# Performance work log

Measured on AMD Instinct MI355X. Metric: run time of the kernel, lower is better.

Reference implementation:

```python
import jax, jax.numpy as jnp
import numpy as np

SIGMA = 10
POPULATIONS = 2
LR = 0.001


def _normalize(L, prior):
    # clamp then normalize over populations (logsumexp across the population axis)
    O = L.shape[1]
    L = jnp.clip(L, -5.0, 0.0)
    lse = jax.nn.logsumexp(L.reshape(POPULATIONS, -1, O), axis=0)  # (in/P, O)
    L = L - jnp.tile(lse, (POPULATIONS, 1))
    prior = jnp.clip(prior, -5.0, 0.0)
    prior = prior - jax.nn.logsumexp(prior)
    return L, prior


def _forward(x, L, prior):
    B, T, IN = x.shape
    O = L.shape[1]
    L, prior = _normalize(L, prior)  # matches normalize_probs() in __init__

    # membrane potential: OR of spikes over trailing window of SIGMA steps
    xb = x.astype(bool)
    pot = xb
    for s in range(1, SIGMA):  # fixed small loop (sigma=10)
        pot = pot | jnp.pad(xb, ((0, 0), (s, 0), (0, 0)))[:, :T, :]

    tpre0 = jnp.full((B, IN), -T, dtype=jnp.int32)
    tpost0 = jnp.full((B, O), jnp.iinfo(jnp.int32).max, dtype=jnp.int32)
    base_key = jax.random.key(42)

    pot_T = jnp.transpose(pot, (1, 0, 2))  # (T,B,IN)
    x_T = jnp.transpose(xb, (1, 0, 2))

    def step(carry, inp):
        L, prior, tpre, tpost, t = carry
        pot_t, x_t = inp
        potf = pot_t.astype(L.dtype)
        logits = potf @ L + prior  # (B,O), logits <= 0 so exp is safe
        # torch: softmax(exp(logits)).multinomial == categorical with logits=exp(logits)
        key = jax.random.fold_in(base_key, t)
        widx = jax.random.categorical(key, jnp.exp(logits), axis=-1)  # (B,)
        win = jax.nn.one_hot(widx, O, dtype=L.dtype)
        # trace updates happen BEFORE STDP, as in the torch code
        tpre = jnp.where(x_t, 0, tpre - 1)
        tpost = jnp.where(win > 0, 0, tpost - 1)
        ltp = (tpre >= -SIGMA).astype(L.dtype)
        ltd = (tpre < -SIGMA).astype(L.dtype)
        post = (tpost < 0).astype(L.dtype)
        m_ltp = jnp.einsum('bi,bo->io', ltp, win) / B
        m_ltd = jnp.einsum('bi,bo->io', ltd, win) / B
        m_pp = jnp.einsum('bi,bo->io', potf, post) / B
        decay = (t + 1).astype(L.dtype)  # lr_decay_inverse starts at 1
        # dw = (5 e^{-L} - 1) * LTP.mean - LTD.mean - pre_post.mean ; LTD was negated
        dw = (5.0 * jnp.exp(-L) - 1.0) * m_ltp + m_ltd - m_pp
        L2 = L + (LR / decay) * dw
        wm = jnp.mean(win, axis=0)
        db = (-5.0 * prior - 1.0) * wm - (1.0 - wm)
        p2 = prior + (LR / decay) * db
        L2, p2 = _normalize(L2, p2)
        return (L2, p2, tpre, tpost, t + 1), None

    (Lf, pf, _, _, _), _ = jax.lax.scan(
        step, (L, prior, tpre0, tpost0, jnp.int32(0)), (pot_T, x_T))
    return jnp.concatenate([Lf.reshape(-1), pf])


def setup_inputs() -> dict:
    key = jax.random.key(0)
    k1, k2, k3 = jax.random.split(key, 3)
    B, T, IN, O = 256, 200, 1568, 100
    x = jax.random.randint(k1, (B, T, IN), 0, 2, dtype=jnp.int32)
    log_likelihood = jax.random.uniform(k2, (IN, O), dtype=jnp.float32) * -1.0 - 1.0
    log_prior = jax.random.uniform(k3, (O,), dtype=jnp.float32) * -1.0 - 1.0
    return {"x": x, "log_likelihood": log_likelihood, "log_prior": log_prior}


def reference(x, log_likelihood, log_prior):
    return _forward(x, log_likelihood, log_prior)
```

## Files before the change

kernel.cpp:

```cpp
#include <hip/hip_runtime.h>
#include <stdint.h>

#define BB 256
#define TT 200
#define INN 1568
#define OO 100
#define PAIRS 784
#define NHALF 12800
#define NBLK 240
#define UNITS 686
#define ROWSTRIDE (4 * INN)

typedef unsigned long long u64;
typedef __attribute__((ext_vector_type(4))) int v4i;

typedef const __attribute__((address_space(1))) uint32_t* gas_p;
typedef __attribute__((address_space(3))) uint32_t* las_p;
#define GLD16(g, l) __builtin_amdgcn_global_load_lds((gas_p)(g), (las_p)(l), 16, 0, 0)

__device__ __forceinline__ void tf_round(uint32_t& x0, uint32_t& x1, int r) {
    x0 += x1;
    x1 = (x1 << r) | (x1 >> (32 - r));
    x1 ^= x0;
}

__device__ __forceinline__ void threefry(uint32_t k0, uint32_t k1,
                                         uint32_t x0, uint32_t x1,
                                         uint32_t& o0, uint32_t& o1) {
    uint32_t k2 = k0 ^ k1 ^ 0x1BD11BDAu;
    x0 += k0; x1 += k1;
    tf_round(x0,x1,13); tf_round(x0,x1,15); tf_round(x0,x1,26); tf_round(x0,x1,6);
    x0 += k1; x1 += k2 + 1u;
    tf_round(x0,x1,17); tf_round(x0,x1,29); tf_round(x0,x1,16); tf_round(x0,x1,24);
    x0 += k2; x1 += k0 + 2u;
    tf_round(x0,x1,13); tf_round(x0,x1,15); tf_round(x0,x1,26); tf_round(x0,x1,6);
    x0 += k0; x1 += k1 + 3u;
    tf_round(x0,x1,17); tf_round(x0,x1,29); tf_round(x0,x1,16); tf_round(x0,x1,24);
    x0 += k1; x1 += k2 + 4u;
    tf_round(x0,x1,13); tf_round(x0,x1,15); tf_round(x0,x1,26); tf_round(x0,x1,6);
    o0 = x0 + k2; o1 = x1 + k0 + 5u;
}

struct FusedSM {
    u64 rows[8][16][64];
    u64 wp[8][8][128];
    u64 potC[8][2][8][10];
    u64 ltpC[8][2][8][10];
    uint32_t cntR[8][8][16];
};
struct FwSM { uint32_t wl32[TT * 65]; int fwl[BB]; };
union SMem { FusedSM f; FwSM w; };

__device__ __forceinline__ void gridsync(uint32_t* c) {
    __syncthreads();
    if (threadIdx.x == 0) {
        __threadfence();
        __hip_atomic_fetch_add(c, 1u, __ATOMIC_ACQ_REL, __HIP_MEMORY_SCOPE_AGENT);
        while (__hip_atomic_load(c, __ATOMIC_ACQUIRE, __HIP_MEMORY_SCOPE_AGENT)
               < (uint32_t)NBLK)
            __builtin_amdgcn_s_sleep(8);
        __threadfence();
    }
    __syncthreads();
}

__global__ __launch_bounds__(512, 1) void k_mono(
        const int* __restrict__ x,
        const float* __restrict__ L0,
        const float* __restrict__ p0arr,
        uint32_t* __restrict__ syncc,
        uint8_t* __restrict__ widx,
        uint32_t* __restrict__ cntg,
        u64* __restrict__ winbits,
        u64* __restrict__ postbits,
        u64* __restrict__ bitB,
        float* __restrict__ outL,
        float* __restrict__ outp) {
    __shared__ SMem sm;
    __shared__ uint32_t smclaim;
    const int tid = threadIdx.x;
    const int bid = blockIdx.x;

    {
        int idx = bid * 214 + tid;
        if (tid < 214 && idx < TT * BB) {
            int t = idx >> 8, b = idx & 255;
            uint32_t fk0, fk1;
            threefry(0u, 42u, 0u, (uint32_t)t, fk0, fk1);
            uint32_t bestkey = 0u;
            int bo = 0;
            int nbase = b * OO;
            for (int o = 0; o < OO; ++o) {
                uint32_t n = (uint32_t)(nbase + o);
                uint32_t lo = (n < NHALF) ? n : n - NHALF;
                uint32_t v0, v1;
                threefry(fk0, fk1, lo, lo + NHALF, v0, v1);
                uint32_t bits = (n < NHALF) ? v0 : v1;
                uint32_t key = bits >> 9;
                if (key > bestkey) { bestkey = key; bo = o; }
            }
            widx[idx] = (uint8_t)bo;
        }
    }
    gridsync(&syncc[0]);

    if (bid < 100) {
        const uint32_t* wsrc = (const uint32_t*)widx;
        for (int g = tid; g < TT * 64; g += 512)
            sm.w.wl32[(g >> 6) * 65 + (g & 63)] = wsrc[g];
        __syncthreads();
        int o = bid;
        if (tid < 64) {
            int f0 = 255, f1 = 255, f2 = 255, f3 = 255;
            for (int t = 0; t < TT; ++t) {
                uint32_t w4 = sm.w.wl32[t * 65 + tid];
                if (((w4      ) & 255u) == (uint32_t)o && f0 == 255) f0 = t;
                if (((w4 >>  8) & 255u) == (uint32_t)o && f1 == 255) f1 = t;
                if (((w4 >> 16) & 255u) == (uint32_t)o && f2 == 255) f2 = t;
                if (((w4 >> 24) & 255u) == (uint32_t)o && f3 == 255) f3 = t;
            }
            sm.w.fwl[4 * tid + 0] = f0; sm.w.fwl[4 * tid + 1] = f1;
            sm.w.fwl[4 * tid + 2] = f2; sm.w.fwl[4 * tid + 3] = f3;
        }
        __syncthreads();
        if (tid < TT) {
            int t = tid;
            u64 wbA[4], pbA[4];
            uint32_t c = 0;
            #pragma unroll
            for (int k = 0; k < 4; ++k) {
                u64 wacc = 0, pacc = 0;
                for (int q2 = 0; q2 < 16; ++q2) {
                    uint32_t w4 = sm.w.wl32[t * 65 + k * 16 + q2];
                    #pragma unroll
                    for (int j = 0; j < 4; ++j) {
                        int bl = q2 * 4 + j;
                        bool win = (((w4 >> (8 * j)) & 255u) == (uint32_t)o);
                        c += win ? 1u : 0u;
                        bool post = (sm.w.fwl[k * 64 + q2 * 4 + j] < t) && !win;
                        u64 bit = 1ull << bl;
                        if (win)  wacc |= bit;
                        if (post) pacc |= bit;
                    }
                }
                wbA[k] = wacc; pbA[k] = pacc;
            }
            size_t base = (size_t)(t * OO + o) * 4;
            #pragma unroll
            for (int k = 0; k < 4; ++k) {
                winbits[base + k] = wbA[k];
                postbits[base + k] = pbA[k];
            }
            cntg[t * OO + o] = c;
        }
        __syncthreads();
    }

    {
        const v4i* xp = (const v4i*)x;
        for (;;) {
            __syncthreads();
            if (tid == 0)
                smclaim = __hip_atomic_fetch_add(&syncc[2], 1u, __ATOMIC_RELAXED,
                                                 __HIP_MEMORY_SCOPE_AGENT);
            __syncthreads();
            uint32_t u = smclaim;
            if (u >= 200u) break;
            int wb = u & 3, tc = u >> 2;
            u64 acc[4][4];
            #pragma unroll
            for (int q = 0; q < 4; ++q)
                #pragma unroll
                for (int c = 0; c < 4; ++c) acc[q][c] = 0;
            bool x4 = (tid < 32);
            for (int blb = 0; blb < 64; blb += 4) {
                v4i v[4][3];
                v4i vt[4];
                #pragma unroll
                for (int s4 = 0; s4 < 4; ++s4) {
                    size_t base = ((size_t)((wb * 64 + blb + s4) * TT + tc * 4)) * 392;
                    #pragma unroll
                    for (int q = 0; q < 3; ++q)
                        v[s4][q] = __builtin_nontemporal_load(&xp[base + tid + q * 512]);
                    if (x4)
                        vt[s4] = __builtin_nontemporal_load(&xp[base + tid + 1536]);
                }
                #pragma unroll
                for (int s4 = 0; s4 < 4; ++s4) {
                    u64 bit = 1ull << (blb + s4);
                    #pragma unroll
                    for (int q = 0; q < 3; ++q) {
                        if (v[s4][q].x) acc[q][0] |= bit;
                        if (v[s4][q].y) acc[q][1] |= bit;
                        if (v[s4][q].z) acc[q][2] |= bit;
                        if (v[s4][q].w) acc[q][3] |= bit;
                    }
                    if (x4) {
                        if (vt[s4].x) acc[3][0] |= bit;
                        if (vt[s4].y) acc[3][1] |= bit;
                        if (vt[s4].z) acc[3][2] |= bit;
                        if (vt[s4].w) acc[3][3] |= bit;
                    }
                }
            }
            #pragma unroll
            for (int q = 0; q < 4; ++q) {
                if (q == 3 && !x4) continue;
                int p = tid + q * 512;
                int tp = (p >= 1176) ? 3 : (p >= 784) ? 2 : (p >= 392) ? 1 : 0;
                int iq = p - tp * 392;
                u64* dst = bitB + ((size_t)((tc * 4 + tp) * 4 + wb)) * INN + iq * 4;
                dst[0] = acc[q][0]; dst[1] = acc[q][1];
                dst[2] = acc[q][2]; dst[3] = acc[q][3];
            }
        }
    }
    gridsync(&syncc[1]);

    {
        const int wv = tid >> 6, lane = tid & 63;
        int u = bid + NBLK * wv;
        if (u > UNITS) return;
        if (u == UNITS) {
            int l = lane;
            bool has2 = (l + 64) < OO;
            float pa = p0arr[l];
            float pb = has2 ? p0arr[l + 64] : -1e30f;
            auto norm = [&]() {
                pa = fminf(fmaxf(pa, -5.0f), 0.0f);
                if (has2) pb = fminf(fmaxf(pb, -5.0f), 0.0f);
                float mx = has2 ? fmaxf(pa, pb) : pa;
                #pragma unroll
                for (int s = 32; s > 0; s >>= 1) mx = fmaxf(mx, __shfl_xor(mx, s, 64));
                float smv = expf(pa - mx) + (has2 ? expf(pb - mx) : 0.0f);
                #pragma unroll
                for (int s = 32; s > 0; s >>= 1) smv += __shfl_xor(smv, s, 64);
                float lse = logf(smv) + mx;
                pa -= lse;
                if (has2) pb -= lse;
            };
            norm();
            for (int t = 0; t < TT; ++t) {
                float eta = 0.001f / (float)(t + 1);
                float wma = (float)cntg[t * OO + l] * (1.0f / 256.0f);
                pa += eta * ((-5.0f * pa - 1.0f) * wma - (1.0f - wma));
                if (has2) {
                    float wmb = (float)cntg[t * OO + l + 64] * (1.0f / 256.0f);
                    pb += eta * ((-5.0f * pb - 1.0f) * wmb - (1.0f - wmb));
                }
                norm();
            }
            outp[l] = pa;
            if (has2) outp[l + 64] = pb;
            return;
        }

        const int pg = u % 98, og = u / 98;
        const int p0 = pg * 8, o0 = og * 16;
        const int pl = lane & 7, ol = lane >> 3;
        const int oA = o0 + ol, oB = oA + 8;
        const int i0 = p0 + pl, i1 = i0 + PAIRS;
        const bool actA = (oA < OO), actB = (oB < OO);

        const int e0 = (lane & 31) * 2;
        const int wk0 = e0 >> 3, wpl0 = e0 & 7;
        const u64* rowg = bitB + (size_t)((wk0 & 3) * INN + (wk0 >> 2) * PAIRS
                                          + p0 + wpl0);
        const int lw = lane & 31;
        const u64* wpg = (lane < 32) ? winbits : postbits;
        const bool wpact = (o0 + (lw >> 1)) < OO;
        const bool cntact = (lane < 8) && ((o0 + (lane & 3) * 4) < OO);

        auto issueG = [&](int G) {
            int r0 = 2 * G;
            {
                int rr = r0 + (lane >> 5); if (rr > TT - 1) rr = TT - 1;
                GLD16(rowg + (size_t)rr * ROWSTRIDE,
                      (las_p)&sm.f.rows[wv][r0 & 15][0]);
            }
            {
                int rr = r0; if (rr > TT - 1) rr = TT - 1;
                if (wpact)
                    GLD16(wpg + ((size_t)rr * OO + o0) * 4 + 2 * lw,
                          (las_p)&sm.f.wp[wv][r0 & 7][0]);
            }
            {
                int rr = r0 + 1; if (rr > TT - 1) rr = TT - 1;
                if (wpact)
                    GLD16(wpg + ((size_t)rr * OO + o0) * 4 + 2 * lw,
                          (las_p)&sm.f.wp[wv][(r0 + 1) & 7][0]);
            }
            {
                if (cntact) {
                    int rr = r0 + (lane >> 2); if (rr > TT - 1) rr = TT - 1;
                    GLD16(cntg + (size_t)rr * OO + o0 + (lane & 3) * 4,
                          (las_p)&sm.f.cntR[wv][r0 & 7][0]);
                }
            }
        };

        float aA = actA ? L0[(size_t)i0 * OO + oA] : -1.0f;
        float bA = actA ? L0[(size_t)i1 * OO + oA] : -1.0f;
        float aB = actB ? L0[(size_t)i0 * OO + oB] : -1.0f;
        float bB = actB ? L0[(size_t)i1 * OO + oB] : -1.0f;
        {
            aA = fminf(fmaxf(aA, -5.0f), 0.0f);
            bA = fminf(fmaxf(bA, -5.0f), 0.0f);
            float m = fmaxf(aA, bA), mn = fminf(aA, bA);
            float lse = __logf(1.0f + __expf(mn - m)) + m;
            aA -= lse; bA -= lse;
            aB = fminf(fmaxf(aB, -5.0f), 0.0f);
            bB = fminf(fmaxf(bB, -5.0f), 0.0f);
            float m2 = fmaxf(aB, bB), mn2 = fminf(aB, bB);
            float lse2 = __logf(1.0f + __expf(mn2 - m2)) + m2;
            aB -= lse2; bB -= lse2;
        }

        auto chainstep = [&](int t, int sp) {
            int s = t & 7;
            const u64* wpS = &sm.f.wp[wv][s][0];
            const u64* P = sm.f.potC[wv][sp][pl];
            const u64* Lt = sm.f.ltpC[wv][sp][pl];
            u64 P0 = P[0], P1 = P[1], P2 = P[2], P3 = P[3];
            u64 P4 = P[4], P5 = P[5], P6 = P[6], P7 = P[7];
            u64 Q0 = Lt[0], Q1 = Lt[1], Q2 = Lt[2], Q3 = Lt[3];
            u64 Q4 = Lt[4], Q5 = Lt[5], Q6 = Lt[6], Q7 = Lt[7];
            float eta = 0.001f / (float)(t + 1);
            {
                u64 W0 = wpS[ol*4+0], W1 = wpS[ol*4+1], W2 = wpS[ol*4+2], W3 = wpS[ol*4+3];
                u64 S0 = wpS[64+ol*4+0], S1 = wpS[64+ol*4+1], S2 = wpS[64+ol*4+2], S3 = wpS[64+ol*4+3];
                float cw = (float)sm.f.cntR[wv][s][ol];
                float lt0 = (float)(__popcll(Q0&W0)+__popcll(Q1&W1)+__popcll(Q2&W2)+__popcll(Q3&W3));
                float lt1 = (float)(__popcll(Q4&W0)+__popcll(Q5&W1)+__popcll(Q6&W2)+__popcll(Q7&W3));
                float pp0 = (float)(__popcll(P0&S0)+__popcll(P1&S1)+__popcll(P2&S2)+__popcll(P3&S3));
                float pp1 = (float)(__popcll(P4&S0)+__popcll(P5&S1)+__popcll(P6&S2)+__popcll(P7&S3));
                float dw0 = (5.0f*__expf(-aA) - 1.0f)*(lt0*(1.0f/256.0f))
                          + (cw - lt0 - pp0)*(1.0f/256.0f);
                float dw1 = (5.0f*__expf(-bA) - 1.0f)*(lt1*(1.0f/256.0f))
                          + (cw - lt1 - pp1)*(1.0f/256.0f);
                aA += eta*dw0; bA += eta*dw1;
                aA = fminf(fmaxf(aA,-5.0f),0.0f);
                bA = fminf(fmaxf(bA,-5.0f),0.0f);
                float m = fmaxf(aA,bA), mn = fminf(aA,bA);
                float lse = __logf(1.0f + __expf(mn-m)) + m;
                aA -= lse; bA -= lse;
            }
            {
                u64 W0 = wpS[(ol+8)*4+0], W1 = wpS[(ol+8)*4+1], W2 = wpS[(ol+8)*4+2], W3 = wpS[(ol+8)*4+3];
                u64 S0 = wpS[64+(ol+8)*4+0], S1 = wpS[64+(ol+8)*4+1], S2 = wpS[64+(ol+8)*4+2], S3 = wpS[64+(ol+8)*4+3];
                float cw = (float)sm.f.cntR[wv][s][ol+8];
                float lt0 = (float)(__popcll(Q0&W0)+__popcll(Q1&W1)+__popcll(Q2&W2)+__popcll(Q3&W3));
                float lt1 = (float)(__popcll(Q4&W0)+__popcll(Q5&W1)+__popcll(Q6&W2)+__popcll(Q7&W3));
                float pp0 = (float)(__popcll(P0&S0)+__popcll(P1&S1)+__popcll(P2&S2)+__popcll(P3&S3));
                float pp1 = (float)(__popcll(P4&S0)+__popcll(P5&S1)+__popcll(P6&S2)+__popcll(P7&S3));
                float dw0 = (5.0f*__expf(-aB) - 1.0f)*(lt0*(1.0f/256.0f))
                          + (cw - lt0 - pp0)*(1.0f/256.0f);
                float dw1 = (5.0f*__expf(-bB) - 1.0f)*(lt1*(1.0f/256.0f))
                          + (cw - lt1 - pp1)*(1.0f/256.0f);
                aB += eta*dw0; bB += eta*dw1;
                aB = fminf(fmaxf(aB,-5.0f),0.0f);
                bB = fminf(fmaxf(bB,-5.0f),0.0f);
                float m = fmaxf(aB,bB), mn = fminf(aB,bB);
                float lse = __logf(1.0f + __expf(mn-m)) + m;
                aB -= lse; bB -= lse;
            }
        };

        issueG(0);
        issueG(1);
        for (int I = 0; I < 100; ++I) {
            issueG(I + 2);
            asm volatile("s_waitcnt vmcnt(8)" ::: "memory");
            int b0 = 2 * I;
            u64 com = 0;
            #pragma unroll
            for (int j = 8; j >= 0; --j) {
                int r = b0 - j; r = (r < 0) ? 0 : r;
                com |= sm.f.rows[wv][r & 15][lane];
            }
            int r9 = b0 - 9;   r9 = (r9 < 0) ? 0 : r9;
            int r10 = b0 - 10; r10 = (r10 < 0) ? 0 : r10;
            u64 v9  = sm.f.rows[wv][r9 & 15][lane];
            u64 v10 = sm.f.rows[wv][r10 & 15][lane];
            u64 vt2 = sm.f.rows[wv][(b0 + 1) & 15][lane];
            u64 pot1 = com | v9;
            u64 pot2 = com | vt2;
            sm.f.potC[wv][0][lane & 7][lane >> 3] = pot1;
            sm.f.potC[wv][1][lane & 7][lane >> 3] = pot2;
            sm.f.ltpC[wv][0][lane & 7][lane >> 3] = pot1 | v10;
            sm.f.ltpC[wv][1][lane & 7][lane >> 3] = pot2 | v9;
            asm volatile("s_waitcnt lgkmcnt(0)" ::: "memory");
            chainstep(b0, 0);
            chainstep(b0 + 1, 1);
        }
        if (actA) {
            outL[(size_t)i0 * OO + oA] = aA;
            outL[(size_t)i1 * OO + oA] = bA;
        }
        if (actB) {
            outL[(size_t)i0 * OO + oB] = aB;
            outL[(size_t)i1 * OO + oB] = bB;
        }
    }
}

extern "C" void kernel_launch(void* const* d_in, const int* in_sizes, int n_in,
                              void* d_out, int out_size, void* d_ws, size_t ws_size,
                              hipStream_t stream) {
    const int*   x  = (const int*)d_in[0];
    const float* L0 = (const float*)d_in[1];
    const float* p0 = (const float*)d_in[2];
    float* out = (float*)d_out;

    char* ws = (char*)d_ws;
    size_t off = 0;
    auto alloc = [&](size_t bytes) -> void* {
        off = (off + 255) & ~(size_t)255;
        void* p = ws + off;
        off += bytes;
        return p;
    };
    uint32_t* syncc    = (uint32_t*)alloc(256);
    uint8_t*  widx     = (uint8_t*) alloc((size_t)TT * BB);
    uint32_t* cntg     = (uint32_t*)alloc((size_t)TT * OO * 4);
    u64*      winbits  = (u64*)     alloc((size_t)TT * OO * 4 * 8);
    u64*      postbits = (u64*)     alloc((size_t)TT * OO * 4 * 8);
    u64*      bitB     = (u64*)     alloc((size_t)TT * 4 * INN * 8);
    (void)ws_size;

    hipMemsetAsync(syncc, 0, 256, stream);
    hipLaunchKernelGGL(k_mono, dim3(NBLK), dim3(512), 0, stream,
                       x, L0, p0, syncc, widx, cntg, winbits, postbits, bitB,
                       out, out + (size_t)INN * OO);
}
```

Before: 689.1 us.

## Restructure STDP chain phase to one element per thread with dedicated loader wave

```diff
diff --git a/kernel.cpp b/kernel.cpp
--- a/kernel.cpp
+++ b/kernel.cpp
@@ -8,7 +8,6 @@
 #define PAIRS 784
 #define NHALF 12800
 #define NBLK 240
-#define UNITS 686
 #define ROWSTRIDE (4 * INN)
 
 typedef unsigned long long u64;
@@ -41,23 +40,24 @@
     o0 = x0 + k2; o1 = x1 + k0 + 5u;
 }
 
-struct FusedSM {
-    u64 rows[8][16][64];
-    u64 wp[8][8][128];
-    u64 potC[8][2][8][10];
-    u64 ltpC[8][2][8][10];
-    uint32_t cntR[8][8][16];
+struct DSM {
+    u64 rowsR[32][128];
+    u64 winR[8][128];
+    u64 postR[8][128];
+    uint32_t cntR[8][32];
+    u64 potC[2][16][10];
+    u64 ltpC[2][16][10];
 };
 struct FwSM { uint32_t wl32[TT * 65]; int fwl[BB]; };
-union SMem { FusedSM f; FwSM w; };
-
-__device__ __forceinline__ void gridsync(uint32_t* c) {
+union SMem { DSM d; FwSM w; };
+
+__device__ __forceinline__ void gridsync(uint32_t* c, uint32_t target) {
     __syncthreads();
     if (threadIdx.x == 0) {
         __threadfence();
         __hip_atomic_fetch_add(c, 1u, __ATOMIC_ACQ_REL, __HIP_MEMORY_SCOPE_AGENT);
         while (__hip_atomic_load(c, __ATOMIC_ACQUIRE, __HIP_MEMORY_SCOPE_AGENT)
-               < (uint32_t)NBLK)
+               < target)
             __builtin_amdgcn_s_sleep(8);
         __threadfence();
     }
@@ -81,9 +81,9 @@
     const int tid = threadIdx.x;
     const int bid = blockIdx.x;
 
-    {
-        int idx = bid * 214 + tid;
-        if (tid < 214 && idx < TT * BB) {
+    if (bid < 100) {
+        {
+            int idx = bid * 512 + tid;
             int t = idx >> 8, b = idx & 255;
             uint32_t fk0, fk1;
             threefry(0u, 42u, 0u, (uint32_t)t, fk0, fk1);
@@ -101,59 +101,58 @@
             }
             widx[idx] = (uint8_t)bo;
         }
-    }
-    gridsync(&syncc[0]);
-
-    if (bid < 100) {
-        const uint32_t* wsrc = (const uint32_t*)widx;
-        for (int g = tid; g < TT * 64; g += 512)
-            sm.w.wl32[(g >> 6) * 65 + (g & 63)] = wsrc[g];
-        __syncthreads();
-        int o = bid;
-        if (tid < 64) {
-            int f0 = 255, f1 = 255, f2 = 255, f3 = 255;
-            for (int t = 0; t < TT; ++t) {
-                uint32_t w4 = sm.w.wl32[t * 65 + tid];
-                if (((w4      ) & 255u) == (uint32_t)o && f0 == 255) f0 = t;
-                if (((w4 >>  8) & 255u) == (uint32_t)o && f1 == 255) f1 = t;
-                if (((w4 >> 16) & 255u) == (uint32_t)o && f2 == 255) f2 = t;
-                if (((w4 >> 24) & 255u) == (uint32_t)o && f3 == 255) f3 = t;
-            }
-            sm.w.fwl[4 * tid + 0] = f0; sm.w.fwl[4 * tid + 1] = f1;
-            sm.w.fwl[4 * tid + 2] = f2; sm.w.fwl[4 * tid + 3] = f3;
-        }
-        __syncthreads();
-        if (tid < TT) {
-            int t = tid;
-            u64 wbA[4], pbA[4];
-            uint32_t c = 0;
-            #pragma unroll
-            for (int k = 0; k < 4; ++k) {
-                u64 wacc = 0, pacc = 0;
-                for (int q2 = 0; q2 < 16; ++q2) {
-                    uint32_t w4 = sm.w.wl32[t * 65 + k * 16 + q2];
-                    #pragma unroll
-                    for (int j = 0; j < 4; ++j) {
-                        int bl = q2 * 4 + j;
-                        bool win = (((w4 >> (8 * j)) & 255u) == (uint32_t)o);
-                        c += win ? 1u : 0u;
-                        bool post = (sm.w.fwl[k * 64 + q2 * 4 + j] < t) && !win;
-                        u64 bit = 1ull << bl;
-                        if (win)  wacc |= bit;
-                        if (post) pacc |= bit;
+        gridsync(&syncc[0], 100u);
+        {
+            const uint32_t* wsrc = (const uint32_t*)widx;
+            for (int g = tid; g < TT * 64; g += 512)
+                sm.w.wl32[(g >> 6) * 65 + (g & 63)] = wsrc[g];
+            __syncthreads();
+            int o = bid;
+            if (tid < 64) {
+                int f0 = 255, f1 = 255, f2 = 255, f3 = 255;
+                for (int t = 0; t < TT; ++t) {
+                    uint32_t w4 = sm.w.wl32[t * 65 + tid];
+                    if (((w4      ) & 255u) == (uint32_t)o && f0 == 255) f0 = t;
+                    if (((w4 >>  8) & 255u) == (uint32_t)o && f1 == 255) f1 = t;
+                    if (((w4 >> 16) & 255u) == (uint32_t)o && f2 == 255) f2 = t;
+                    if (((w4 >> 24) & 255u) == (uint32_t)o && f3 == 255) f3 = t;
+                }
+                sm.w.fwl[4 * tid + 0] = f0; sm.w.fwl[4 * tid + 1] = f1;
+                sm.w.fwl[4 * tid + 2] = f2; sm.w.fwl[4 * tid + 3] = f3;
+            }
+            __syncthreads();
+            if (tid < TT) {
+                int t = tid;
+                u64 wbA[4], pbA[4];
+                uint32_t c = 0;
+                #pragma unroll
+                for (int k = 0; k < 4; ++k) {
+                    u64 wacc = 0, pacc = 0;
+                    for (int q2 = 0; q2 < 16; ++q2) {
+                        uint32_t w4 = sm.w.wl32[t * 65 + k * 16 + q2];
+                        #pragma unroll
+                        for (int j = 0; j < 4; ++j) {
+                            int bl = q2 * 4 + j;
+                            bool win = (((w4 >> (8 * j)) & 255u) == (uint32_t)o);
+                            c += win ? 1u : 0u;
+                            bool post = (sm.w.fwl[k * 64 + q2 * 4 + j] < t) && !win;
+                            u64 bit = 1ull << bl;
+                            if (win)  wacc |= bit;
+                            if (post) pacc |= bit;
+                        }
                     }
+                    wbA[k] = wacc; pbA[k] = pacc;
                 }
-                wbA[k] = wacc; pbA[k] = pacc;
-            }
-            size_t base = (size_t)(t * OO + o) * 4;
-            #pragma unroll
-            for (int k = 0; k < 4; ++k) {
-                winbits[base + k] = wbA[k];
-                postbits[base + k] = pbA[k];
-            }
-            cntg[t * OO + o] = c;
-        }
-        __syncthreads();
+                size_t base = (size_t)(t * OO + o) * 4;
+                #pragma unroll
+                for (int k = 0; k < 4; ++k) {
+                    winbits[base + k] = wbA[k];
+                    postbits[base + k] = pbA[k];
+                }
+                cntg[t * OO + o] = c;
+            }
+            __syncthreads();
+        }
     }
 
     {
@@ -215,192 +214,158 @@
             }
         }
     }
-    gridsync(&syncc[1]);
-
-    {
-        const int wv = tid >> 6, lane = tid & 63;
-        int u = bid + NBLK * wv;
-        if (u > UNITS) return;
-        if (u == UNITS) {
-            int l = lane;
-            bool has2 = (l + 64) < OO;
-            float pa = p0arr[l];
-            float pb = has2 ? p0arr[l + 64] : -1e30f;
-            auto norm = [&]() {
-                pa = fminf(fmaxf(pa, -5.0f), 0.0f);
-                if (has2) pb = fminf(fmaxf(pb, -5.0f), 0.0f);
-                float mx = has2 ? fmaxf(pa, pb) : pa;
-                #pragma unroll
-                for (int s = 32; s > 0; s >>= 1) mx = fmaxf(mx, __shfl_xor(mx, s, 64));
-                float smv = expf(pa - mx) + (has2 ? expf(pb - mx) : 0.0f);
-                #pragma unroll
-                for (int s = 32; s > 0; s >>= 1) smv += __shfl_xor(smv, s, 64);
-                float lse = logf(smv) + mx;
-                pa -= lse;
-                if (has2) pb -= lse;
-            };
+    gridsync(&syncc[1], (uint32_t)NBLK);
+
+    if (bid >= 197) return;
+    if (bid == 196) {
+        if (tid >= 64) return;
+        int l = tid;
+        bool has2 = (l + 64) < OO;
+        float pa = p0arr[l];
+        float pb = has2 ? p0arr[l + 64] : -1e30f;
+        auto norm = [&]() {
+            pa = fminf(fmaxf(pa, -5.0f), 0.0f);
+            if (has2) pb = fminf(fmaxf(pb, -5.0f), 0.0f);
+            float mx = has2 ? fmaxf(pa, pb) : pa;
+            #pragma unroll
+            for (int s = 32; s > 0; s >>= 1) mx = fmaxf(mx, __shfl_xor(mx, s, 64));
+            float smv = expf(pa - mx) + (has2 ? expf(pb - mx) : 0.0f);
+            #pragma unroll
+            for (int s = 32; s > 0; s >>= 1) smv += __shfl_xor(smv, s, 64);
+            float lse = logf(smv) + mx;
+            pa -= lse;
+            if (has2) pb -= lse;
+        };
+        norm();
+        uint32_t na = cntg[l];
+        uint32_t nb = has2 ? cntg[l + 64] : 0u;
+        for (int t = 0; t < TT; ++t) {
+            float ca = (float)na, cb = (float)nb;
+            if (t < TT - 1) {
+                na = cntg[(t + 1) * OO + l];
+                nb = has2 ? cntg[(t + 1) * OO + l + 64] : 0u;
+            }
+            float eta = 0.001f / (float)(t + 1);
+            float wma = ca * (1.0f / 256.0f);
+            pa += eta * ((-5.0f * pa - 1.0f) * wma - (1.0f - wma));
+            if (has2) {
+                float wmb = cb * (1.0f / 256.0f);
+                pb += eta * ((-5.0f * pb - 1.0f) * wmb - (1.0f - wmb));
+            }
             norm();
-            for (int t = 0; t < TT; ++t) {
-                float eta = 0.001f / (float)(t + 1);
-                float wma = (float)cntg[t * OO + l] * (1.0f / 256.0f);
-                pa += eta * ((-5.0f * pa - 1.0f) * wma - (1.0f - wma));
-                if (has2) {
-                    float wmb = (float)cntg[t * OO + l + 64] * (1.0f / 256.0f);
-                    pb += eta * ((-5.0f * pb - 1.0f) * wmb - (1.0f - wmb));
-                }
-                norm();
-            }
-            outp[l] = pa;
-            if (has2) outp[l + 64] = pb;
-            return;
-        }
-
-        const int pg = u % 98, og = u / 98;
-        const int p0 = pg * 8, o0 = og * 16;
-        const int pl = lane & 7, ol = lane >> 3;
-        const int oA = o0 + ol, oB = oA + 8;
-        const int i0 = p0 + pl, i1 = i0 + PAIRS;
-        const bool actA = (oA < OO), actB = (oB < OO);
-
-        const int e0 = (lane & 31) * 2;
-        const int wk0 = e0 >> 3, wpl0 = e0 & 7;
-        const u64* rowg = bitB + (size_t)((wk0 & 3) * INN + (wk0 >> 2) * PAIRS
-                                          + p0 + wpl0);
-        const int lw = lane & 31;
-        const u64* wpg = (lane < 32) ? winbits : postbits;
-        const bool wpact = (o0 + (lw >> 1)) < OO;
-        const bool cntact = (lane < 8) && ((o0 + (lane & 3) * 4) < OO);
-
-        auto issueG = [&](int G) {
-            int r0 = 2 * G;
-            {
-                int rr = r0 + (lane >> 5); if (rr > TT - 1) rr = TT - 1;
-                GLD16(rowg + (size_t)rr * ROWSTRIDE,
-                      (las_p)&sm.f.rows[wv][r0 & 15][0]);
-            }
-            {
-                int rr = r0; if (rr > TT - 1) rr = TT - 1;
-                if (wpact)
-                    GLD16(wpg + ((size_t)rr * OO + o0) * 4 + 2 * lw,
-                          (las_p)&sm.f.wp[wv][r0 & 7][0]);
-            }
-            {
-                int rr = r0 + 1; if (rr > TT - 1) rr = TT - 1;
-                if (wpact)
-                    GLD16(wpg + ((size_t)rr * OO + o0) * 4 + 2 * lw,
-                          (las_p)&sm.f.wp[wv][(r0 + 1) & 7][0]);
-            }
-            {
-                if (cntact) {
-                    int rr = r0 + (lane >> 2); if (rr > TT - 1) rr = TT - 1;
-                    GLD16(cntg + (size_t)rr * OO + o0 + (lane & 3) * 4,
-                          (las_p)&sm.f.cntR[wv][r0 & 7][0]);
-                }
-            }
-        };
-
-        float aA = actA ? L0[(size_t)i0 * OO + oA] : -1.0f;
-        float bA = actA ? L0[(size_t)i1 * OO + oA] : -1.0f;
-        float aB = actB ? L0[(size_t)i0 * OO + oB] : -1.0f;
-        float bB = actB ? L0[(size_t)i1 * OO + oB] : -1.0f;
-        {
-            aA = fminf(fmaxf(aA, -5.0f), 0.0f);
-            bA = fminf(fmaxf(bA, -5.0f), 0.0f);
-            float m = fmaxf(aA, bA), mn = fminf(aA, bA);
+        }
+        outp[l] = pa;
+        if (has2) outp[l + 64] = pb;
+        return;
+    }
+
+    const int og = bid / 49, pg = bid % 49;
+    const int o0 = og * 25, p0 = pg * 16;
+    const int pl = tid & 15, olx = tid >> 4;
+    const bool isChain = (tid < 400);
+    const int o  = o0 + olx;
+    const int i0 = p0 + pl, i1 = i0 + PAIRS;
+    const int wave = tid >> 6, ll = tid & 63;
+    const bool isLoader = (wave == 7);
+
+    const int wk0 = ll >> 3, wpl0 = (ll & 7) * 2;
+    const u64* rowg = bitB + (size_t)((wk0 & 3) * INN + (wk0 >> 2) * PAIRS
+                                      + p0 + wpl0);
+    auto issue = [&](int G) {
+        #pragma unroll
+        for (int h = 0; h < 2; ++h) {
+            int s = 2 * G + h;
+            int rr = (s < TT) ? s : (TT - 1);
+            GLD16(rowg + (size_t)rr * ROWSTRIDE, (las_p)&sm.d.rowsR[s & 31][2 * ll]);
+            if (ll < 50) {
+                GLD16(winbits + ((size_t)rr * OO + o0) * 4 + 2 * ll,
+                      (las_p)&sm.d.winR[s & 7][2 * ll]);
+                GLD16(postbits + ((size_t)rr * OO + o0) * 4 + 2 * ll,
+                      (las_p)&sm.d.postR[s & 7][2 * ll]);
+            }
+            if (ll < 7)
+                GLD16(cntg + (size_t)rr * OO + o0 + 4 * ll,
+                      (las_p)&sm.d.cntR[s & 7][4 * ll]);
+        }
+    };
+
+    if (isLoader) {
+        issue(0); issue(1); issue(2);
+        asm volatile("s_waitcnt vmcnt(0)" ::: "memory");
+    }
+    __builtin_amdgcn_s_barrier();
+    if (tid < 128) {
+        int k = tid >> 4, plq = tid & 15;
+        u64 r0 = sm.d.rowsR[0][k * 16 + plq];
+        sm.d.potC[0][plq][k] = r0;
+        sm.d.ltpC[0][plq][k] = r0;
+    }
+    float a = -1.0f, b2 = -1.0f;
+    if (isChain) {
+        a  = L0[(size_t)i0 * OO + o];
+        b2 = L0[(size_t)i1 * OO + o];
+        a  = fminf(fmaxf(a,  -5.0f), 0.0f);
+        b2 = fminf(fmaxf(b2, -5.0f), 0.0f);
+        float m = fmaxf(a, b2), mn = fminf(a, b2);
+        float lse = __logf(1.0f + __expf(mn - m)) + m;
+        a -= lse; b2 -= lse;
+    }
+    asm volatile("s_waitcnt lgkmcnt(0)" ::: "memory");
+    __builtin_amdgcn_s_barrier();
+
+    for (int t = 0; t < TT; ++t) {
+        int cur = t & 1, nxt = cur ^ 1;
+        if (isLoader && (t & 1) == 0) issue(t / 2 + 3);
+        if (isChain) {
+            const u64* W = &sm.d.winR[t & 7][olx * 4];
+            const u64* S = &sm.d.postR[t & 7][olx * 4];
+            const u64* P = sm.d.potC[cur][pl];
+            const u64* Q = sm.d.ltpC[cur][pl];
+            float cw = (float)sm.d.cntR[t & 7][olx];
+            float lt0 = (float)(__popcll(Q[0]&W[0]) + __popcll(Q[1]&W[1])
+                              + __popcll(Q[2]&W[2]) + __popcll(Q[3]&W[3]));
+            float lt1 = (float)(__popcll(Q[4]&W[0]) + __popcll(Q[5]&W[1])
+                              + __popcll(Q[6]&W[2]) + __popcll(Q[7]&W[3]));
+            float pp0 = (float)(__popcll(P[0]&S[0]) + __popcll(P[1]&S[1])
+                              + __popcll(P[2]&S[2]) + __popcll(P[3]&S[3]));
+            float pp1 = (float)(__popcll(P[4]&S[0]) + __popcll(P[5]&S[1])
+                              + __popcll(P[6]&S[2]) + __popcll(P[7]&S[3]));
+            float eta = 0.001f / (float)(t + 1);
+            float dw0 = (5.0f * __expf(-a)  - 1.0f) * (lt0 * (1.0f/256.0f))
+                      + (cw - lt0 - pp0) * (1.0f/256.0f);
+            float dw1 = (5.0f * __expf(-b2) - 1.0f) * (lt1 * (1.0f/256.0f))
+                      + (cw - lt1 - pp1) * (1.0f/256.0f);
+            a  += eta * dw0;
+            b2 += eta * dw1;
+            a  = fminf(fmaxf(a,  -5.0f), 0.0f);
+            b2 = fminf(fmaxf(b2, -5.0f), 0.0f);
+            float m = fmaxf(a, b2), mn = fminf(a, b2);
             float lse = __logf(1.0f + __expf(mn - m)) + m;
-            aA -= lse; bA -= lse;
-            aB = fminf(fmaxf(aB, -5.0f), 0.0f);
-            bB = fminf(fmaxf(bB, -5.0f), 0.0f);
-            float m2 = fmaxf(aB, bB), mn2 = fminf(aB, bB);
-            float lse2 = __logf(1.0f + __expf(mn2 - m2)) + m2;
-            aB -= lse2; bB -= lse2;
-        }
-
-        auto chainstep = [&](int t, int sp) {
-            int s = t & 7;
-            const u64* wpS = &sm.f.wp[wv][s][0];
-            const u64* P = sm.f.potC[wv][sp][pl];
-            const u64* Lt = sm.f.ltpC[wv][sp][pl];
-            u64 P0 = P[0], P1 = P[1], P2 = P[2], P3 = P[3];
-            u64 P4 = P[4], P5 = P[5], P6 = P[6], P7 = P[7];
-            u64 Q0 = Lt[0], Q1 = Lt[1], Q2 = Lt[2], Q3 = Lt[3];
-            u64 Q4 = Lt[4], Q5 = Lt[5], Q6 = Lt[6], Q7 = Lt[7];
-            float eta = 0.001f / (float)(t + 1);
-            {
-                u64 W0 = wpS[ol*4+0], W1 = wpS[ol*4+1], W2 = wpS[ol*4+2], W3 = wpS[ol*4+3];
-                u64 S0 = wpS[64+ol*4+0], S1 = wpS[64+ol*4+1], S2 = wpS[64+ol*4+2], S3 = wpS[64+ol*4+3];
-                float cw = (float)sm.f.cntR[wv][s][ol];
-                float lt0 = (float)(__popcll(Q0&W0)+__popcll(Q1&W1)+__popcll(Q2&W2)+__popcll(Q3&W3));
-                float lt1 = (float)(__popcll(Q4&W0)+__popcll(Q5&W1)+__popcll(Q6&W2)+__popcll(Q7&W3));
-                float pp0 = (float)(__popcll(P0&S0)+__popcll(P1&S1)+__popcll(P2&S2)+__popcll(P3&S3));
-                float pp1 = (float)(__popcll(P4&S0)+__popcll(P5&S1)+__popcll(P6&S2)+__popcll(P7&S3));
-                float dw0 = (5.0f*__expf(-aA) - 1.0f)*(lt0*(1.0f/256.0f))
-                          + (cw - lt0 - pp0)*(1.0f/256.0f);
-                float dw1 = (5.0f*__expf(-bA) - 1.0f)*(lt1*(1.0f/256.0f))
-                          + (cw - lt1 - pp1)*(1.0f/256.0f);
-                aA += eta*dw0; bA += eta*dw1;
-                aA = fminf(fmaxf(aA,-5.0f),0.0f);
-                bA = fminf(fmaxf(bA,-5.0f),0.0f);
-                float m = fmaxf(aA,bA), mn = fminf(aA,bA);
-                float lse = __logf(1.0f + __expf(mn-m)) + m;
-                aA -= lse; bA -= lse;
-            }
-            {
-                u64 W0 = wpS[(ol+8)*4+0], W1 = wpS[(ol+8)*4+1], W2 = wpS[(ol+8)*4+2], W3 = wpS[(ol+8)*4+3];
-                u64 S0 = wpS[64+(ol+8)*4+0], S1 = wpS[64+(ol+8)*4+1], S2 = wpS[64+(ol+8)*4+2], S3 = wpS[64+(ol+8)*4+3];
-                float cw = (float)sm.f.cntR[wv][s][ol+8];
-                float lt0 = (float)(__popcll(Q0&W0)+__popcll(Q1&W1)+__popcll(Q2&W2)+__popcll(Q3&W3));
-                float lt1 = (float)(__popcll(Q4&W0)+__popcll(Q5&W1)+__popcll(Q6&W2)+__popcll(Q7&W3));
-                float pp0 = (float)(__popcll(P0&S0)+__popcll(P1&S1)+__popcll(P2&S2)+__popcll(P3&S3));
-                float pp1 = (float)(__popcll(P4&S0)+__popcll(P5&S1)+__popcll(P6&S2)+__popcll(P7&S3));
-                float dw0 = (5.0f*__expf(-aB) - 1.0f)*(lt0*(1.0f/256.0f))
-                          + (cw - lt0 - pp0)*(1.0f/256.0f);
-                float dw1 = (5.0f*__expf(-bB) - 1.0f)*(lt1*(1.0f/256.0f))
-                          + (cw - lt1 - pp1)*(1.0f/256.0f);
-                aB += eta*dw0; bB += eta*dw1;
-                aB = fminf(fmaxf(aB,-5.0f),0.0f);
-                bB = fminf(fmaxf(bB,-5.0f),0.0f);
-                float m = fmaxf(aB,bB), mn = fminf(aB,bB);
-                float lse = __logf(1.0f + __expf(mn-m)) + m;
-                aB -= lse; bB -= lse;
-            }
-        };
-
-        issueG(0);
-        issueG(1);
-        for (int I = 0; I < 100; ++I) {
-            issueG(I + 2);
-            asm volatile("s_waitcnt vmcnt(8)" ::: "memory");
-            int b0 = 2 * I;
-            u64 com = 0;
+            a -= lse; b2 -= lse;
+        }
+        if (tid < 128 && t + 1 < TT) {
+            int k = tid >> 4, plq = tid & 15;
+            int e = k * 16 + plq;
+            u64 acc = 0;
             #pragma unroll
-            for (int j = 8; j >= 0; --j) {
-                int r = b0 - j; r = (r < 0) ? 0 : r;
-                com |= sm.f.rows[wv][r & 15][lane];
-            }
-            int r9 = b0 - 9;   r9 = (r9 < 0) ? 0 : r9;
-            int r10 = b0 - 10; r10 = (r10 < 0) ? 0 : r10;
-            u64 v9  = sm.f.rows[wv][r9 & 15][lane];
-            u64 v10 = sm.f.rows[wv][r10 & 15][lane];
-            u64 vt2 = sm.f.rows[wv][(b0 + 1) & 15][lane];
-            u64 pot1 = com | v9;
-            u64 pot2 = com | vt2;
-            sm.f.potC[wv][0][lane & 7][lane >> 3] = pot1;
-            sm.f.potC[wv][1][lane & 7][lane >> 3] = pot2;
-            sm.f.ltpC[wv][0][lane & 7][lane >> 3] = pot1 | v10;
-            sm.f.ltpC[wv][1][lane & 7][lane >> 3] = pot2 | v9;
+            for (int j = 9; j >= 0; --j) {
+                int rr = t + 1 - j; if (rr < 0) rr = 0;
+                acc |= sm.d.rowsR[rr & 31][e];
+            }
+            int rm = t + 1 - 10; if (rm < 0) rm = 0;
+            u64 v10 = sm.d.rowsR[rm & 31][e];
+            sm.d.potC[nxt][plq][k] = acc;
+            sm.d.ltpC[nxt][plq][k] = acc | v10;
+        }
+        if (isLoader)
+            asm volatile("s_waitcnt vmcnt(16) lgkmcnt(0)" ::: "memory");
+        else
             asm volatile("s_waitcnt lgkmcnt(0)" ::: "memory");
-            chainstep(b0, 0);
-            chainstep(b0 + 1, 1);
-        }
-        if (actA) {
-            outL[(size_t)i0 * OO + oA] = aA;
-            outL[(size_t)i1 * OO + oA] = bA;
-        }
-        if (actB) {
-            outL[(size_t)i0 * OO + oB] = aB;
-            outL[(size_t)i1 * OO + oB] = bB;
-        }
+        __builtin_amdgcn_s_barrier();
+    }
+    if (isChain) {
+        outL[(size_t)i0 * OO + o] = a;
+        outL[(size_t)i1 * OO + o] = b2;
     }
 }
 
```

Result: slower. 728.8 us (+5.8%).
